# Optimization experiments

Measured on AMD Instinct MI355X. Metric: run time of the kernel, lower is better.

Reference implementation:

```python
import jax, jax.numpy as jnp
import numpy as np

B, C, T = 64, 512, 1000
BR = 3
RED = 1
H = C // RED


def setup_inputs() -> dict:
    key = jax.random.key(0)
    ks = jax.random.split(key, 8)
    x0 = jax.random.normal(ks[0], (B, C, T), dtype=jnp.float32)
    x1 = jax.random.normal(ks[1], (B, C, T), dtype=jnp.float32)
    x2 = jax.random.normal(ks[2], (B, C, T), dtype=jnp.float32)
    # linear1: Conv1d(2C -> H, kernel 1) == dense [H, 2C]
    W1 = jax.random.normal(ks[3], (H, 2 * C), dtype=jnp.float32) * (1.0 / np.sqrt(2 * C))
    b1 = jnp.zeros((H,), dtype=jnp.float32)
    # linear2: BR branch convs Conv1d(H -> C, kernel 1), stacked: [BR, C, H]
    W2 = jax.random.normal(ks[4], (BR, C, H), dtype=jnp.float32) * (1.0 / np.sqrt(H))
    b2 = jnp.zeros((BR, C), dtype=jnp.float32)
    return {"x0": x0, "x1": x1, "x2": x2, "W1": W1, "b1": b1, "W2": W2, "b2": b2}


def reference(x0, x1, x2, W1, b1, W2, b2):
    # f: [B, BR, C, T]
    f = jnp.stack([x0, x1, x2], axis=1)
    xs = f.sum(axis=1)  # [B, C, T]
    t = xs.shape[-1]
    mean = xs.mean(axis=-1)  # [B, C]
    # unbiased std (torch.std default)
    var = ((xs - mean[..., None]) ** 2).sum(axis=-1) / (t - 1)
    std = jnp.sqrt(var)
    stats = jnp.concatenate([mean, std], axis=-1)  # [B, 2C]
    h = stats @ W1.T + b1  # [B, H]
    s = jnp.einsum('bh,kch->bkc', h, W2) + b2  # [B, BR, C]
    w = jax.nn.softmax(s, axis=1)[..., None]  # [B, BR, C, 1]
    return (f * w).sum(axis=1)  # [B, C, T]
```

## Files before the change

### kernel.cpp

```cpp
#include <hip/hip_runtime.h>
#include <math.h>

#define NB 64
#define NC 512
#define NT 1000
#define NH 512
#define TWOC 1024
#define NT4 250

__global__ __launch_bounds__(256) void stats_kernel(const float* __restrict__ x0,
                                                    const float* __restrict__ x1,
                                                    const float* __restrict__ x2,
                                                    float* __restrict__ stats) {
    const int row  = blockIdx.x;
    const int tid  = threadIdx.x;
    const int lane = tid & 63;
    const int wave = tid >> 6;

    float s = 0.f, sq = 0.f;
    if (tid < NT4) {
        const int idx = row * NT4 + tid;
        const float4 a = ((const float4*)x0)[idx];
        const float4 d = ((const float4*)x1)[idx];
        const float4 e = ((const float4*)x2)[idx];
        const float v0 = a.x + d.x + e.x;
        const float v1 = a.y + d.y + e.y;
        const float v2 = a.z + d.z + e.z;
        const float v3 = a.w + d.w + e.w;
        s  = v0 + v1 + v2 + v3;
        sq = v0*v0 + v1*v1 + v2*v2 + v3*v3;
    }
    #pragma unroll
    for (int off = 32; off; off >>= 1) {
        s  += __shfl_down(s,  off);
        sq += __shfl_down(sq, off);
    }
    __shared__ float ps[4], pq[4];
    if (lane == 0) { ps[wave] = s; pq[wave] = sq; }
    __syncthreads();
    if (tid == 0) {
        const float S = ps[0] + ps[1] + ps[2] + ps[3];
        const float Q = pq[0] + pq[1] + pq[2] + pq[3];
        const float mean = S / (float)NT;
        const float var  = (Q - S * S / (float)NT) / (float)(NT - 1);
        const float sd   = sqrtf(fmaxf(var, 0.f));
        const int b = row >> 9;
        const int c = row & (NC - 1);
        stats[b * TWOC + c]      = mean;
        stats[b * TWOC + NC + c] = sd;
    }
}

__global__ __launch_bounds__(256) void h_kernel(const float* __restrict__ stats,
                                                const float* __restrict__ W1,
                                                const float* __restrict__ b1,
                                                float* __restrict__ hbuf) {
    const int wid  = blockIdx.x * 4 + (threadIdx.x >> 6);
    const int lane = threadIdx.x & 63;
    const int j    = wid >> 4;
    const int b0   = (wid & 15) * 4;

    const float4* wr = (const float4*)(W1 + (size_t)j * TWOC);
    const float4* s0p = (const float4*)(stats + (size_t)(b0 + 0) * TWOC);
    const float4* s1p = (const float4*)(stats + (size_t)(b0 + 1) * TWOC);
    const float4* s2p = (const float4*)(stats + (size_t)(b0 + 2) * TWOC);
    const float4* s3p = (const float4*)(stats + (size_t)(b0 + 3) * TWOC);

    float a0 = 0.f, a1 = 0.f, a2 = 0.f, a3 = 0.f;
    #pragma unroll
    for (int r = 0; r < 4; ++r) {
        const int i4 = r * 64 + lane;
        const float4 wv = wr[i4];
        const float4 v0 = s0p[i4];
        const float4 v1 = s1p[i4];
        const float4 v2 = s2p[i4];
        const float4 v3 = s3p[i4];
        a0 += wv.x*v0.x + wv.y*v0.y + wv.z*v0.z + wv.w*v0.w;
        a1 += wv.x*v1.x + wv.y*v1.y + wv.z*v1.z + wv.w*v1.w;
        a2 += wv.x*v2.x + wv.y*v2.y + wv.z*v2.z + wv.w*v2.w;
        a3 += wv.x*v3.x + wv.y*v3.y + wv.z*v3.z + wv.w*v3.w;
    }
    #pragma unroll
    for (int off = 32; off; off >>= 1) {
        a0 += __shfl_down(a0, off);
        a1 += __shfl_down(a1, off);
        a2 += __shfl_down(a2, off);
        a3 += __shfl_down(a3, off);
    }
    if (lane == 0) {
        const float bb = b1[j];
        hbuf[(size_t)(b0 + 0) * NH + j] = a0 + bb;
        hbuf[(size_t)(b0 + 1) * NH + j] = a1 + bb;
        hbuf[(size_t)(b0 + 2) * NH + j] = a2 + bb;
        hbuf[(size_t)(b0 + 3) * NH + j] = a3 + bb;
    }
}

__global__ __launch_bounds__(256) void sw_kernel(const float* __restrict__ hbuf,
                                                 const float* __restrict__ W2,
                                                 const float* __restrict__ b2,
                                                 float* __restrict__ wbuf) {
    const int wid  = blockIdx.x * 4 + (threadIdx.x >> 6);
    const int lane = threadIdx.x & 63;
    const int c    = wid >> 4;
    const int b0   = (wid & 15) * 4;

    const float4* w0r = (const float4*)(W2 + ((size_t)(0 * NC + c)) * NH);
    const float4* w1r = (const float4*)(W2 + ((size_t)(1 * NC + c)) * NH);
    const float4* w2r = (const float4*)(W2 + ((size_t)(2 * NC + c)) * NH);

    float acc00=0,acc01=0,acc02=0,acc03=0;
    float acc10=0,acc11=0,acc12=0,acc13=0;
    float acc20=0,acc21=0,acc22=0,acc23=0;

    #pragma unroll
    for (int r = 0; r < 2; ++r) {
        const int i4 = r * 64 + lane;
        const float4 w0v = w0r[i4];
        const float4 w1v = w1r[i4];
        const float4 w2v = w2r[i4];
        const float4 h0 = ((const float4*)(hbuf + (size_t)(b0 + 0) * NH))[i4];
        const float4 h1 = ((const float4*)(hbuf + (size_t)(b0 + 1) * NH))[i4];
        const float4 h2 = ((const float4*)(hbuf + (size_t)(b0 + 2) * NH))[i4];
        const float4 h3 = ((const float4*)(hbuf + (size_t)(b0 + 3) * NH))[i4];
        acc00 += w0v.x*h0.x + w0v.y*h0.y + w0v.z*h0.z + w0v.w*h0.w;
        acc01 += w0v.x*h1.x + w0v.y*h1.y + w0v.z*h1.z + w0v.w*h1.w;
        acc02 += w0v.x*h2.x + w0v.y*h2.y + w0v.z*h2.z + w0v.w*h2.w;
        acc03 += w0v.x*h3.x + w0v.y*h3.y + w0v.z*h3.z + w0v.w*h3.w;
        acc10 += w1v.x*h0.x + w1v.y*h0.y + w1v.z*h0.z + w1v.w*h0.w;
        acc11 += w1v.x*h1.x + w1v.y*h1.y + w1v.z*h1.z + w1v.w*h1.w;
        acc12 += w1v.x*h2.x + w1v.y*h2.y + w1v.z*h2.z + w1v.w*h2.w;
        acc13 += w1v.x*h3.x + w1v.y*h3.y + w1v.z*h3.z + w1v.w*h3.w;
        acc20 += w2v.x*h0.x + w2v.y*h0.y + w2v.z*h0.z + w2v.w*h0.w;
        acc21 += w2v.x*h1.x + w2v.y*h1.y + w2v.z*h1.z + w2v.w*h1.w;
        acc22 += w2v.x*h2.x + w2v.y*h2.y + w2v.z*h2.z + w2v.w*h2.w;
        acc23 += w2v.x*h3.x + w2v.y*h3.y + w2v.z*h3.z + w2v.w*h3.w;
    }
    #pragma unroll
    for (int off = 32; off; off >>= 1) {
        acc00 += __shfl_down(acc00, off); acc01 += __shfl_down(acc01, off);
        acc02 += __shfl_down(acc02, off); acc03 += __shfl_down(acc03, off);
        acc10 += __shfl_down(acc10, off); acc11 += __shfl_down(acc11, off);
        acc12 += __shfl_down(acc12, off); acc13 += __shfl_down(acc13, off);
        acc20 += __shfl_down(acc20, off); acc21 += __shfl_down(acc21, off);
        acc22 += __shfl_down(acc22, off); acc23 += __shfl_down(acc23, off);
    }
    if (lane == 0) {
        const float bb0 = b2[0 * NC + c];
        const float bb1 = b2[1 * NC + c];
        const float bb2 = b2[2 * NC + c];
        float v0[4] = {acc00 + bb0, acc01 + bb0, acc02 + bb0, acc03 + bb0};
        float v1[4] = {acc10 + bb1, acc11 + bb1, acc12 + bb1, acc13 + bb1};
        float v2[4] = {acc20 + bb2, acc21 + bb2, acc22 + bb2, acc23 + bb2};
        #pragma unroll
        for (int bb = 0; bb < 4; ++bb) {
            const float m  = fmaxf(v0[bb], fmaxf(v1[bb], v2[bb]));
            const float e0 = expf(v0[bb] - m);
            const float e1 = expf(v1[bb] - m);
            const float e2 = expf(v2[bb] - m);
            const float inv = 1.f / (e0 + e1 + e2);
            const size_t base = (size_t)(b0 + bb) * 3 * NC + c;
            wbuf[base + 0 * NC] = e0 * inv;
            wbuf[base + 1 * NC] = e1 * inv;
            wbuf[base + 2 * NC] = e2 * inv;
        }
    }
}

__global__ __launch_bounds__(256) void apply_kernel(const float* __restrict__ x0,
                                                    const float* __restrict__ x1,
                                                    const float* __restrict__ x2,
                                                    const float* __restrict__ wbuf,
                                                    float* __restrict__ out) {
    const int row = blockIdx.x;
    const int tid = threadIdx.x;
    if (tid >= NT4) return;
    const int b = row >> 9;
    const int c = row & (NC - 1);
    const float w0 = wbuf[((size_t)b * 3 + 0) * NC + c];
    const float w1 = wbuf[((size_t)b * 3 + 1) * NC + c];
    const float w2 = wbuf[((size_t)b * 3 + 2) * NC + c];
    const int idx = row * NT4 + tid;
    const float4 a = ((const float4*)x0)[idx];
    const float4 d = ((const float4*)x1)[idx];
    const float4 e = ((const float4*)x2)[idx];
    float4 r;
    r.x = a.x*w0 + d.x*w1 + e.x*w2;
    r.y = a.y*w0 + d.y*w1 + e.y*w2;
    r.z = a.z*w0 + d.z*w1 + e.z*w2;
    r.w = a.w*w0 + d.w*w1 + e.w*w2;
    ((float4*)out)[idx] = r;
}

extern "C" void kernel_launch(void* const* d_in, const int* in_sizes, int n_in,
                              void* d_out, int out_size, void* d_ws, size_t ws_size,
                              hipStream_t stream) {
    const float* x0 = (const float*)d_in[0];
    const float* x1 = (const float*)d_in[1];
    const float* x2 = (const float*)d_in[2];
    const float* W1 = (const float*)d_in[3];
    const float* b1 = (const float*)d_in[4];
    const float* W2 = (const float*)d_in[5];
    const float* b2 = (const float*)d_in[6];
    float* out = (float*)d_out;

    float* stats = (float*)d_ws;
    float* hbuf  = stats + NB * TWOC;
    float* wbuf  = hbuf + NB * NH;

    stats_kernel<<<NB * NC, 256, 0, stream>>>(x0, x1, x2, stats);
    h_kernel<<<2048, 256, 0, stream>>>(stats, W1, b1, hbuf);
    sw_kernel<<<2048, 256, 0, stream>>>(hbuf, W2, b2, wbuf);
    apply_kernel<<<NB * NC, 256, 0, stream>>>(x0, x1, x2, wbuf, out);
}
```

Measured before the change: 193.9 us.

## Map one wavefront per row in stats and apply kernels

Stats and apply kernels now assign each (b,c) row to a single 64-lane wavefront that loops over four float4 chunks, instead of one 256-thread block per row. This removes the idle threads past 250 in each block and the shared-memory plus __syncthreads cross-wave reduction in stats, and cuts the grid size by four. Each lane now holds more loads in flight, which costs extra registers, and the last chunk needs a lane-masked tail.

```diff
diff --git a/kernel.cpp b/kernel.cpp
--- a/kernel.cpp
+++ b/kernel.cpp
@@ -7,42 +7,61 @@
 #define NH 512
 #define TWOC 1024
 #define NT4 250
+#define TAIL 58
 
 __global__ __launch_bounds__(256) void stats_kernel(const float* __restrict__ x0,
                                                     const float* __restrict__ x1,
                                                     const float* __restrict__ x2,
                                                     float* __restrict__ stats) {
-    const int row  = blockIdx.x;
-    const int tid  = threadIdx.x;
-    const int lane = tid & 63;
-    const int wave = tid >> 6;
+    const int row  = blockIdx.x * 4 + (threadIdx.x >> 6);
+    const int lane = threadIdx.x & 63;
+
+    const float4* p0 = (const float4*)x0 + (size_t)row * NT4;
+    const float4* p1 = (const float4*)x1 + (size_t)row * NT4;
+    const float4* p2 = (const float4*)x2 + (size_t)row * NT4;
+
+    const float4 a0 = p0[lane];       const float4 a1 = p0[lane + 64];
+    const float4 a2 = p0[lane + 128];
+    const float4 b0 = p1[lane];       const float4 b1 = p1[lane + 64];
+    const float4 b2 = p1[lane + 128];
+    const float4 c0 = p2[lane];       const float4 c1 = p2[lane + 64];
+    const float4 c2 = p2[lane + 128];
+    float4 a3 = {0,0,0,0}, b3 = {0,0,0,0}, c3 = {0,0,0,0};
+    if (lane < TAIL) {
+        a3 = p0[lane + 192];
+        b3 = p1[lane + 192];
+        c3 = p2[lane + 192];
+    }
 
     float s = 0.f, sq = 0.f;
-    if (tid < NT4) {
-        const int idx = row * NT4 + tid;
-        const float4 a = ((const float4*)x0)[idx];
-        const float4 d = ((const float4*)x1)[idx];
-        const float4 e = ((const float4*)x2)[idx];
-        const float v0 = a.x + d.x + e.x;
-        const float v1 = a.y + d.y + e.y;
-        const float v2 = a.z + d.z + e.z;
-        const float v3 = a.w + d.w + e.w;
-        s  = v0 + v1 + v2 + v3;
-        sq = v0*v0 + v1*v1 + v2*v2 + v3*v3;
-    }
+    {
+        float v;
+        v = a0.x + b0.x + c0.x; s += v; sq += v * v;
+        v = a0.y + b0.y + c0.y; s += v; sq += v * v;
+        v = a0.z + b0.z + c0.z; s += v; sq += v * v;
+        v = a0.w + b0.w + c0.w; s += v; sq += v * v;
+        v = a1.x + b1.x + c1.x; s += v; sq += v * v;
+        v = a1.y + b1.y + c1.y; s += v; sq += v * v;
+        v = a1.z + b1.z + c1.z; s += v; sq += v * v;
+        v = a1.w + b1.w + c1.w; s += v; sq += v * v;
+        v = a2.x + b2.x + c2.x; s += v; sq += v * v;
+        v = a2.y + b2.y + c2.y; s += v; sq += v * v;
+        v = a2.z + b2.z + c2.z; s += v; sq += v * v;
+        v = a2.w + b2.w + c2.w; s += v; sq += v * v;
+        v = a3.x + b3.x + c3.x; s += v; sq += v * v;
+        v = a3.y + b3.y + c3.y; s += v; sq += v * v;
+        v = a3.z + b3.z + c3.z; s += v; sq += v * v;
+        v = a3.w + b3.w + c3.w; s += v; sq += v * v;
+    }
+
     #pragma unroll
     for (int off = 32; off; off >>= 1) {
         s  += __shfl_down(s,  off);
         sq += __shfl_down(sq, off);
     }
-    __shared__ float ps[4], pq[4];
-    if (lane == 0) { ps[wave] = s; pq[wave] = sq; }
-    __syncthreads();
-    if (tid == 0) {
-        const float S = ps[0] + ps[1] + ps[2] + ps[3];
-        const float Q = pq[0] + pq[1] + pq[2] + pq[3];
-        const float mean = S / (float)NT;
-        const float var  = (Q - S * S / (float)NT) / (float)(NT - 1);
+    if (lane == 0) {
+        const float mean = s / (float)NT;
+        const float var  = (sq - s * s / (float)NT) / (float)(NT - 1);
         const float sd   = sqrtf(fmaxf(var, 0.f));
         const int b = row >> 9;
         const int c = row & (NC - 1);
@@ -60,7 +79,7 @@
     const int j    = wid >> 4;
     const int b0   = (wid & 15) * 4;
 
-    const float4* wr = (const float4*)(W1 + (size_t)j * TWOC);
+    const float4* wr  = (const float4*)(W1 + (size_t)j * TWOC);
     const float4* s0p = (const float4*)(stats + (size_t)(b0 + 0) * TWOC);
     const float4* s1p = (const float4*)(stats + (size_t)(b0 + 1) * TWOC);
     const float4* s2p = (const float4*)(stats + (size_t)(b0 + 2) * TWOC);
@@ -172,24 +191,44 @@
                                                     const float* __restrict__ x2,
                                                     const float* __restrict__ wbuf,
                                                     float* __restrict__ out) {
-    const int row = blockIdx.x;
-    const int tid = threadIdx.x;
-    if (tid >= NT4) return;
+    const int row  = blockIdx.x * 4 + (threadIdx.x >> 6);
+    const int lane = threadIdx.x & 63;
     const int b = row >> 9;
     const int c = row & (NC - 1);
     const float w0 = wbuf[((size_t)b * 3 + 0) * NC + c];
     const float w1 = wbuf[((size_t)b * 3 + 1) * NC + c];
     const float w2 = wbuf[((size_t)b * 3 + 2) * NC + c];
-    const int idx = row * NT4 + tid;
-    const float4 a = ((const float4*)x0)[idx];
-    const float4 d = ((const float4*)x1)[idx];
-    const float4 e = ((const float4*)x2)[idx];
-    float4 r;
-    r.x = a.x*w0 + d.x*w1 + e.x*w2;
-    r.y = a.y*w0 + d.y*w1 + e.y*w2;
-    r.z = a.z*w0 + d.z*w1 + e.z*w2;
-    r.w = a.w*w0 + d.w*w1 + e.w*w2;
-    ((float4*)out)[idx] = r;
+
+    const float4* p0 = (const float4*)x0 + (size_t)row * NT4;
+    const float4* p1 = (const float4*)x1 + (size_t)row * NT4;
+    const float4* p2 = (const float4*)x2 + (size_t)row * NT4;
+    float4*       po = (float4*)out      + (size_t)row * NT4;
+
+    #pragma unroll
+    for (int r = 0; r < 3; ++r) {
+        const int i = r * 64 + lane;
+        const float4 a = p0[i];
+        const float4 d = p1[i];
+        const float4 e = p2[i];
+        float4 o;
+        o.x = a.x*w0 + d.x*w1 + e.x*w2;
+        o.y = a.y*w0 + d.y*w1 + e.y*w2;
+        o.z = a.z*w0 + d.z*w1 + e.z*w2;
+        o.w = a.w*w0 + d.w*w1 + e.w*w2;
+        po[i] = o;
+    }
+    if (lane < TAIL) {
+        const int i = 192 + lane;
+        const float4 a = p0[i];
+        const float4 d = p1[i];
+        const float4 e = p2[i];
+        float4 o;
+        o.x = a.x*w0 + d.x*w1 + e.x*w2;
+        o.y = a.y*w0 + d.y*w1 + e.y*w2;
+        o.z = a.z*w0 + d.z*w1 + e.z*w2;
+        o.w = a.w*w0 + d.w*w1 + e.w*w2;
+        po[i] = o;
+    }
 }
 
 extern "C" void kernel_launch(void* const* d_in, const int* in_sizes, int n_in,
@@ -208,8 +247,8 @@
     float* hbuf  = stats + NB * TWOC;
     float* wbuf  = hbuf + NB * NH;
 
-    stats_kernel<<<NB * NC, 256, 0, stream>>>(x0, x1, x2, stats);
+    stats_kernel<<<NB * NC / 4, 256, 0, stream>>>(x0, x1, x2, stats);
     h_kernel<<<2048, 256, 0, stream>>>(stats, W1, b1, hbuf);
     sw_kernel<<<2048, 256, 0, stream>>>(hbuf, W2, b2, wbuf);
-    apply_kernel<<<NB * NC, 256, 0, stream>>>(x0, x1, x2, wbuf, out);
-}
+    apply_kernel<<<NB * NC / 4, 256, 0, stream>>>(x0, x1, x2, wbuf, out);
+}
```

New measurement: 199.7 us. 1.03x slower.
